# Optimization experiments

Measured on AMD Instinct MI355X. Metric: run time of the kernel, lower is better.

The kernel has to match this reference:

```python
import jax, jax.numpy as jnp
import numpy as np

D = 300   # hidden dim (Linear(300,300))
L = 160   # seq len, forced by W3 = Linear(160,1)


def _linear(x, W, b):
    # torch Linear: x @ W.T + b, W is (out, in)
    return jnp.matmul(x, W.T) + b


def setup_inputs() -> dict:
    key = jax.random.key(0)
    ks = jax.random.split(key, 16)
    B = 1024
    s = 1.0 / np.sqrt(D)
    inp = {
        'T_feature': jax.random.normal(ks[0], (B, L, D), jnp.float32),
        'CD_feature': jax.random.normal(ks[1], (B, L, D), jnp.float32),
        'Wproj': jax.random.normal(ks[2], (D, D), jnp.float32) * s,
        'bproj': jnp.zeros((D,), jnp.float32),
        'WqT_w': jax.random.normal(ks[3], (D, D), jnp.float32) * s,
        'WqT_b': jnp.zeros((D,), jnp.float32),
        'WqCD_w': jax.random.normal(ks[4], (D, D), jnp.float32) * s,
        'WqCD_b': jnp.zeros((D,), jnp.float32),
        'WkT_w': jax.random.normal(ks[5], (D, D), jnp.float32) * s,
        'WkT_b': jnp.zeros((D,), jnp.float32),
        'WkCD_w': jax.random.normal(ks[6], (D, D), jnp.float32) * s,
        'WkCD_b': jnp.zeros((D,), jnp.float32),
        'W3_w': jax.random.normal(ks[7], (1, L), jnp.float32) * (1.0 / np.sqrt(L)),
        'W3_b': jnp.zeros((1,), jnp.float32),
    }
    return inp


def reference(T_feature, CD_feature, Wproj, bproj, WqT_w, WqT_b, WqCD_w, WqCD_b,
              WkT_w, WkT_b, WkCD_w, WkCD_b, W3_w, W3_b):
    sqrt_d = jnp.sqrt(jnp.float32(D))
    proj_T = _linear(T_feature, Wproj, bproj)     # (B, L, D)
    proj_CD = _linear(CD_feature, Wproj, bproj)   # (B, L, D)

    # N_tensor @ proj_T is just the mean over tokens (weights 1/Len)
    mean_T = jnp.mean(proj_T, axis=1, keepdims=True)          # (B, 1, D)
    qT = _linear(mean_T, WqT_w, WqT_b)                        # (B, 1, D)
    kT = _linear(proj_T, WkT_w, WkT_b)                        # (B, L, D)
    alphaT = jnp.einsum('bqd,bkd->bqk', qT, kT) / sqrt_d      # (B, 1, L)
    ZT = jax.nn.sigmoid(alphaT)

    qCD = _linear(proj_CD, WqCD_w, WqCD_b)                    # (B, L, D)
    kCD = _linear(proj_CD, WkCD_w, WkCD_b)                    # (B, L, D)
    alphaCD = jnp.einsum('bqd,bkd->bqk', qCD, kCD) / sqrt_d   # (B, L, L)
    ZCD = jax.nn.sigmoid(alphaCD)

    # The per-token loop+cat is a plain broadcast multiply: Mt[:,i,:] = ZCD[:,i,:] * ZT[:,0,:]
    Mt = ZCD * ZT                                             # (B, L, L)
    alpha_f = jax.nn.softmax(_linear(Mt, W3_w, W3_b), axis=1) # (B, L, 1)

    # Second loop is a per-token scalar scale: HCD[:,i,:] = alpha_f[:,i,0] * proj_CD[:,i,:]
    HCD = alpha_f * proj_CD                                   # (B, L, D)
    return (proj_T, HCD)
```

## Files before the change

kernel.cpp:

```cpp
#include <hip/hip_runtime.h>
#include <hip/hip_bf16.h>


typedef __attribute__((ext_vector_type(8))) short short8;
typedef __attribute__((ext_vector_type(4))) float f32x4;

#define DP 320

__device__ __forceinline__ unsigned short f2bf(float x) {
  unsigned int u = __builtin_bit_cast(unsigned int, x);
  u += 0x7FFFu + ((u >> 16) & 1u);
  return (unsigned short)(u >> 16);
}
__device__ __forceinline__ float bf2f(unsigned short h) {
  unsigned int u = ((unsigned int)h) << 16;
  return __builtin_bit_cast(float, u);
}
__device__ __forceinline__ void gload16(const void* g, void* l) {
  __builtin_amdgcn_global_load_lds(
      (const __attribute__((address_space(1))) unsigned int*)g,
      (__attribute__((address_space(3))) unsigned int*)l, 16, 0, 0);
}
__device__ __forceinline__ float sigm(float x) { return 1.0f / (1.0f + __expf(-x)); }
__device__ __forceinline__ size_t baddr(int n, int k) {
  return (size_t)(k >> 6) * 20480 + (size_t)(n >> 4) * 1024 + ((k >> 5) & 1) * 512 +
         ((((k >> 3) & 3) << 4) | (n & 15)) * 8 + (k & 7);
}
__device__ __forceinline__ size_t aaddr(size_t r, int k) {
  return ((r >> 4) * 5 + (k >> 6)) * 1024 + ((k >> 5) & 1) * 512 +
         ((((k >> 3) & 3) << 4) | (r & 15)) * 8 + (k & 7);
}

__global__ __launch_bounds__(320)
void prep1_k(const float* __restrict__ W,
             const float* __restrict__ WqCD_w, const float* __restrict__ WqCD_b,
             const float* __restrict__ WkCD_w, const float* __restrict__ WkCD_b,
             const float* __restrict__ WqT_w, const float* __restrict__ WqT_b,
             const float* __restrict__ WkT_w, const float* __restrict__ WkT_b,
             unsigned short* __restrict__ Wb, float* __restrict__ Wt,
             unsigned short* __restrict__ MaugT, float* __restrict__ Pmat,
             float isd) {
  const int x = blockIdx.x, c = threadIdx.x;
  if (x < 320) {
    const int n = x;
    unsigned short v = (n < 300 && c < 300) ? f2bf(W[n * 300 + c]) : (unsigned short)0;
    Wb[baddr(n, c)] = v;
    if (n < 300 && c < 300) Wt[c * 304 + n] = W[n * 300 + c];
  } else if (x < 640) {
    const int n = x - 320;
    float v = 0.f;
    if (n <= 300 && c <= 300) {
      for (int o = 0; o < 300; ++o) {
        float a = (c < 300) ? WqCD_w[o * 300 + c] : WqCD_b[o];
        float b = (n < 300) ? WkCD_w[o * 300 + n] : WkCD_b[o];
        v += a * b;
      }
      v *= isd;
    }
    MaugT[baddr(n, c)] = f2bf(v);
  } else {
    const int n = x - 640;
    float v = 0.f;
    if (n <= 300 && c <= 300) {
      for (int o = 0; o < 300; ++o) {
        float a = (c < 300) ? WkT_w[o * 300 + c] : WkT_b[o];
        float b = (n < 300) ? WqT_w[o * 300 + n] : WqT_b[o];
        v += a * b;
      }
      v *= isd;
    }
    Pmat[n * DP + c] = v;
  }
}

__global__ __launch_bounds__(512)
void gemm_k(const float* __restrict__ Tf, const float* __restrict__ CDf,
            const unsigned short* __restrict__ Ah,
            const unsigned short* __restrict__ B01,
            const unsigned short* __restrict__ B2,
            const float* __restrict__ bias,
            float* __restrict__ Of, unsigned short* __restrict__ pCDout,
            unsigned short* __restrict__ Yout, int mode_base) {
  __shared__ __align__(16) unsigned short As[2][8192];
  __shared__ __align__(16) unsigned short Bs[2][20480];
  const int tid = threadIdx.x, wid = tid >> 6, lane = tid & 63;
  const int lr = lane & 15, hi = lane >> 4;
  const int wr = wid >> 2, wc = wid & 3;
  const int mode = mode_base + blockIdx.y;
  const size_t m0 = (size_t)blockIdx.x * 128;
  const unsigned short* __restrict__ Bm = (mode == 2) ? B2 : B01;
  const float* __restrict__ Af = (mode == 0) ? Tf : CDf;

  f32x4 acc[4][5];
#pragma unroll
  for (int i = 0; i < 4; ++i)
#pragma unroll
    for (int j = 0; j < 5; ++j) acc[i][j] = (f32x4){0.f, 0.f, 0.f, 0.f};

  f32x4 ar[4];
  auto loadA = [&](int kc) {
#pragma unroll
    for (int u = 0; u < 2; ++u) {
      const int unit = tid * 2 + u;
      const int row = unit >> 3, cg = unit & 7;
      const int col0 = kc * 64 + cg * 8;
      const float* p = Af + (m0 + row) * 300 + col0;
      if (col0 + 8 <= 300) {
        ar[u * 2] = *(const f32x4*)p;
        ar[u * 2 + 1] = *(const f32x4*)(p + 4);
      } else {
#pragma unroll
        for (int j = 0; j < 4; ++j) {
          ar[u * 2][j] = (col0 + j < 300) ? p[j] : 0.f;
          ar[u * 2 + 1][j] = (col0 + 4 + j < 300) ? p[4 + j] : 0.f;
        }
      }
    }
  };
  auto writeA = [&](int buf) {
#pragma unroll
    for (int u = 0; u < 2; ++u) {
      const int unit = tid * 2 + u;
      const int row = unit >> 3, cg = unit & 7;
      short8 h;
#pragma unroll
      for (int j = 0; j < 4; ++j) {
        h[j] = (short)f2bf(ar[u * 2][j]);
        h[j + 4] = (short)f2bf(ar[u * 2 + 1][j]);
      }
      *(short8*)&As[buf][(size_t)(row >> 4) * 1024 + (size_t)(cg >> 2) * 512 +
                         ((((cg & 3) << 4) | (row & 15)) * 8)] = h;
    }
  };
  auto stageA2 = [&](int buf, int kc) {
#pragma unroll
    for (int it = 0; it < 2; ++it) {
      int idx = it * 512 + tid;
      gload16(Ah + (((m0 >> 4) + (idx >> 7)) * 5 + kc) * 1024 + (size_t)(idx & 127) * 8,
              (char*)As[buf] + (size_t)idx * 16);
    }
  };
  auto stageB = [&](int buf, int kc) {
#pragma unroll
    for (int it = 0; it < 5; ++it) {
      int idx = it * 512 + tid;
      gload16(Bm + (size_t)kc * 20480 + (size_t)idx * 8, (char*)Bs[buf] + (size_t)idx * 16);
    }
  };

  if (mode < 2) { loadA(0); stageB(0, 0); writeA(0); }
  else { stageA2(0, 0); stageB(0, 0); }
  __syncthreads();

  for (int kc = 0; kc < 5; ++kc) {
    const int cur = kc & 1;
    if (kc < 4) {
      if (mode < 2) loadA(kc + 1);
      else stageA2(cur ^ 1, kc + 1);
      stageB(cur ^ 1, kc + 1);
    }
#pragma unroll
    for (int kk = 0; kk < 2; ++kk) {
      short8 a[4], b[5];
#pragma unroll
      for (int mf = 0; mf < 4; ++mf)
        a[mf] = *(const short8*)&As[cur][(size_t)(wr * 4 + mf) * 1024 + kk * 512 + lane * 8];
#pragma unroll
      for (int nf = 0; nf < 5; ++nf)
        b[nf] = *(const short8*)&Bs[cur][(size_t)(wc * 5 + nf) * 1024 + kk * 512 + lane * 8];
#pragma unroll
      for (int mf = 0; mf < 4; ++mf)
#pragma unroll
        for (int nf = 0; nf < 5; ++nf)
          acc[mf][nf] = __builtin_amdgcn_mfma_f32_16x16x32_bf16(a[mf], b[nf], acc[mf][nf], 0, 0, 0);
    }
    if (kc < 4 && mode < 2) writeA(cur ^ 1);
    __syncthreads();
  }

#pragma unroll
  for (int mf = 0; mf < 4; ++mf) {
    const size_t rowb = m0 + wr * 64 + mf * 16 + hi * 4;
#pragma unroll
    for (int nf = 0; nf < 5; ++nf) {
      const int col = wc * 80 + nf * 16 + lr;
      const float bv = (mode < 2) ? ((col < 300) ? bias[col] : 0.f) : 0.f;
#pragma unroll
      for (int r = 0; r < 4; ++r) {
        const size_t rw = rowb + r;
        float v = acc[mf][nf][r] + bv;
        if (mode == 0) {
          if (col < 300) Of[rw * 300 + col] = v;
        } else if (mode == 1) {
          unsigned short u = (col < 300) ? f2bf(v)
                           : ((col == 300) ? f2bf(1.0f) : (unsigned short)0);
          pCDout[aaddr(rw, col)] = u;
        } else {
          Yout[aaddr(rw, col)] = f2bf(v);
        }
      }
    }
  }
}

__global__ __launch_bounds__(320)
void gate2_k(const float* __restrict__ T, const float* __restrict__ Pmat,
             const float* __restrict__ W, const float* __restrict__ Wt,
             const float* __restrict__ bproj, float* __restrict__ ZT) {
  __shared__ float mt[304];
  __shared__ float maug[304];
  __shared__ float vv[304];
  __shared__ float wt[304];
  __shared__ float cpr;
  const int b = blockIdx.x, t = threadIdx.x;
  const int wid = t >> 6, lane = t & 63;
  const float* Tb = T + (size_t)b * 48000;
  if (t < 300) {
    float s = 0.f;
#pragma unroll 4
    for (int l = 0; l < 160; ++l) s += Tb[l * 300 + t];
    mt[t] = s * (1.0f / 160.0f);
  }
  __syncthreads();
  if (t < 304) {
    if (t < 300) {
      float s = 0.f;
      for (int o = 0; o < 300; ++o) s += Wt[o * 304 + t] * mt[o];
      maug[t] = s + bproj[t];
    } else maug[t] = (t == 300) ? 1.f : 0.f;
  }
  __syncthreads();
  if (t < 304) {
    float s = 0.f;
    if (t <= 300) for (int a = 0; a <= 300; ++a) s += Pmat[a * DP + t] * maug[a];
    vv[t] = s;
  }
  __syncthreads();
  if (t < 304) {
    if (t < 300) {
      float s = 0.f;
      for (int c = 0; c < 300; ++c) s += vv[c] * W[c * 300 + t];
      wt[t] = s;
    } else {
      wt[t] = 0.f;
      if (t == 300) {
        float s = 0.f;
        for (int c = 0; c < 300; ++c) s += vv[c] * bproj[c];
        cpr = s + vv[300];
      }
    }
  }
  __syncthreads();
  for (int j = wid * 32; j < wid * 32 + 32; ++j) {
    const float* row = Tb + j * 300;
    float s = 0.f;
    for (int c = lane; c < 300; c += 64) s += wt[c] * row[c];
#pragma unroll
    for (int m = 1; m < 64; m <<= 1) s += __shfl_xor(s, m, 64);
    if (lane == 0) ZT[b * 160 + j] = sigm(s + cpr);
  }
}

__global__ __launch_bounds__(640)
void finale_k(const unsigned short* __restrict__ Yg, const unsigned short* __restrict__ Pg,
              const float* __restrict__ ZT, const float* __restrict__ W3w,
              float* __restrict__ out) {
  __shared__ __align__(16) unsigned short Ps[51200];
  __shared__ float t_arr[160];
  __shared__ float s_arr[160];
  __shared__ float red0;
  const int b = blockIdx.x, tid = threadIdx.x, wid = tid >> 6, lane = tid & 63;
  const int lr = lane & 15, hi = lane >> 4;
  const unsigned short* Pb = Pg + (size_t)b * 51200;
  const unsigned short* Yb = Yg + (size_t)b * 51200;

  if (tid < 160) t_arr[tid] = ZT[b * 160 + tid] * W3w[tid];

  auto stageP = [&](int kc) {
#pragma unroll
    for (int it = 0; it < 2; ++it) {
      int idx = it * 640 + tid;
      int r16 = idx >> 7, rem = idx & 127;
      gload16(Pb + ((size_t)r16 * 5 + kc) * 1024 + (size_t)rem * 8,
              (char*)Ps + ((size_t)kc * 10240 + (size_t)idx * 8) * 2);
    }
  };
  short8 yf[2][2];
  auto loadY = [&](short8 (&dst)[2], int kc) {
#pragma unroll
    for (int kk = 0; kk < 2; ++kk)
      dst[kk] = *(const short8*)(Yb + ((size_t)wid * 5 + kc) * 1024 + kk * 512 + lane * 8);
  };

  f32x4 acc[10];
#pragma unroll
  for (int j = 0; j < 10; ++j) acc[j] = (f32x4){0.f, 0.f, 0.f, 0.f};

  stageP(0);
  loadY(yf[0], 0);
  __syncthreads();
#pragma unroll
  for (int kc = 0; kc < 5; ++kc) {
    const int cur = kc & 1;
    if (kc < 4) { stageP(kc + 1); loadY(yf[cur ^ 1], kc + 1); }
#pragma unroll
    for (int kk = 0; kk < 2; ++kk)
#pragma unroll
      for (int nf = 0; nf < 10; ++nf) {
        short8 bb = *(const short8*)&Ps[kc * 10240 + nf * 1024 + kk * 512 + lane * 8];
        acc[nf] = __builtin_amdgcn_mfma_f32_16x16x32_bf16(yf[cur][kk], bb, acc[nf], 0, 0, 0);
      }
    __syncthreads();
  }

  float pp[4];
#pragma unroll
  for (int r = 0; r < 4; ++r) {
    float s = 0.f;
#pragma unroll
    for (int nf = 0; nf < 10; ++nf) s += sigm(acc[nf][r]) * t_arr[nf * 16 + lr];
    pp[r] = s;
  }
#pragma unroll
  for (int m = 1; m < 16; m <<= 1)
#pragma unroll
    for (int r = 0; r < 4; ++r) pp[r] += __shfl_xor(pp[r], m, 64);
  if (lr == 0) {
#pragma unroll
    for (int r = 0; r < 4; ++r) s_arr[wid * 16 + hi * 4 + r] = pp[r];
  }
  __syncthreads();
  if (wid == 0) {
    float v0 = s_arr[lane], v1 = s_arr[lane + 64];
    float v2 = (lane < 32) ? s_arr[lane + 128] : -3.0e38f;
    float mx = fmaxf(fmaxf(v0, v1), v2);
#pragma unroll
    for (int m = 1; m < 64; m <<= 1) mx = fmaxf(mx, __shfl_xor(mx, m, 64));
    float e0 = __expf(v0 - mx), e1 = __expf(v1 - mx);
    float e2 = (lane < 32) ? __expf(v2 - mx) : 0.f;
    s_arr[lane] = e0; s_arr[lane + 64] = e1;
    if (lane < 32) s_arr[lane + 128] = e2;
    float sm = e0 + e1 + e2;
#pragma unroll
    for (int m = 1; m < 64; m <<= 1) sm += __shfl_xor(sm, m, 64);
    if (lane == 0) red0 = 1.0f / sm;
  }
  __syncthreads();
  const float inv = red0;
  float* ob = out + (size_t)b * 48000;
#pragma unroll
  for (int it = 0; it < 10; ++it) {
    int idx = it * 640 + tid;
    int i = idx / 40, g = idx - i * 40;
    int c0 = g * 8;
    if (c0 < 300) {
      short8 pv = *(const short8*)&Ps[(g >> 3) * 10240 + (i >> 4) * 1024 +
                                      ((g >> 2) & 1) * 512 + ((((g & 3) << 4) | (i & 15)) * 8)];
      float sc = s_arr[i] * inv;
      if (c0 + 8 <= 300) {
        f32x4 o0, o1;
#pragma unroll
        for (int j = 0; j < 4; ++j) { o0[j] = sc * bf2f((unsigned short)pv[j]); o1[j] = sc * bf2f((unsigned short)pv[j + 4]); }
        *(f32x4*)(ob + (size_t)i * 300 + c0) = o0;
        *(f32x4*)(ob + (size_t)i * 300 + c0 + 4) = o1;
      } else {
#pragma unroll
        for (int j = 0; j < 8; ++j) {
          int c = c0 + j;
          if (c < 300) ob[(size_t)i * 300 + c] = sc * bf2f((unsigned short)pv[j]);
        }
      }
    }
  }
}

extern "C" void kernel_launch(void* const* d_in, const int* in_sizes, int n_in,
                              void* d_out, int out_size, void* d_ws, size_t ws_size,
                              hipStream_t stream) {
  (void)in_sizes; (void)n_in; (void)out_size; (void)ws_size;
  const float* T      = (const float*)d_in[0];
  const float* CD     = (const float*)d_in[1];
  const float* Wproj  = (const float*)d_in[2];
  const float* bproj  = (const float*)d_in[3];
  const float* WqT_w  = (const float*)d_in[4];
  const float* WqT_b  = (const float*)d_in[5];
  const float* WqCD_w = (const float*)d_in[6];
  const float* WqCD_b = (const float*)d_in[7];
  const float* WkT_w  = (const float*)d_in[8];
  const float* WkT_b  = (const float*)d_in[9];
  const float* WkCD_w = (const float*)d_in[10];
  const float* WkCD_b = (const float*)d_in[11];
  const float* W3_w   = (const float*)d_in[12];

  char* ws = (char*)d_ws;
  size_t off = 0;
  auto alloc = [&](size_t bytes) { void* p = ws + off; off = (off + bytes + 255) & ~(size_t)255; return p; };
  unsigned short* Wb    = (unsigned short*)alloc((size_t)DP * DP * 2);
  unsigned short* MaugT = (unsigned short*)alloc((size_t)DP * DP * 2);
  float* Pmat = (float*)alloc((size_t)DP * DP * 4);
  float* Wt   = (float*)alloc((size_t)304 * 304 * 4);
  float* ZT   = (float*)alloc((size_t)1024 * 160 * 4);
  unsigned short* pCDg = (unsigned short*)alloc((size_t)163840 * DP * 2);
  unsigned short* Yg   = (unsigned short*)alloc((size_t)163840 * DP * 2);

  float* projT = (float*)d_out;
  float* HCD   = (float*)d_out + (size_t)49152000;

  const float isd = 1.0f / sqrtf(300.0f);

  prep1_k<<<dim3(960), dim3(320), 0, stream>>>(Wproj, WqCD_w, WqCD_b, WkCD_w, WkCD_b,
                                               WqT_w, WqT_b, WkT_w, WkT_b,
                                               Wb, Wt, MaugT, Pmat, isd);
  gemm_k<<<dim3(1280, 2), dim3(512), 0, stream>>>(T, CD, nullptr, Wb, nullptr,
                                                  bproj, projT, pCDg, nullptr, 0);
  gemm_k<<<dim3(1280, 1), dim3(512), 0, stream>>>(nullptr, nullptr, pCDg, nullptr, MaugT,
                                                  nullptr, nullptr, nullptr, Yg, 2);
  gate2_k<<<dim3(1024), dim3(320), 0, stream>>>(T, Pmat, Wproj, Wt, bproj, ZT);
  finale_k<<<dim3(1024), dim3(640), 0, stream>>>(Yg, pCDg, ZT, W3_w, HCD);
}
```

Measured before the change: 669.8 us.

## Shrink GEMM M-tile to 64 and load A fragments directly into registers

The GEMM block tile drops from 128 to 64 rows and the grid doubles. Each wave now loads its own A fragments straight from global memory into registers in MFMA layout instead of staging A through shared memory. This removes the A LDS buffer and its writes and reads, and sets launch_bounds to 4 blocks per CU to raise occupancy. In exchange, each B tile is reused across half as many rows, so B loads are repeated more often, and the uncoalesced per-lane A loads may waste bandwidth.

```diff
diff --git a/kernel.cpp b/kernel.cpp
--- a/kernel.cpp
+++ b/kernel.cpp
@@ -73,7 +73,7 @@
   }
 }
 
-__global__ __launch_bounds__(512)
+__global__ __launch_bounds__(512, 4)
 void gemm_k(const float* __restrict__ Tf, const float* __restrict__ CDf,
             const unsigned short* __restrict__ Ah,
             const unsigned short* __restrict__ B01,
@@ -81,63 +81,67 @@
             const float* __restrict__ bias,
             float* __restrict__ Of, unsigned short* __restrict__ pCDout,
             unsigned short* __restrict__ Yout, int mode_base) {
-  __shared__ __align__(16) unsigned short As[2][8192];
   __shared__ __align__(16) unsigned short Bs[2][20480];
   const int tid = threadIdx.x, wid = tid >> 6, lane = tid & 63;
   const int lr = lane & 15, hi = lane >> 4;
   const int wr = wid >> 2, wc = wid & 3;
   const int mode = mode_base + blockIdx.y;
-  const size_t m0 = (size_t)blockIdx.x * 128;
+  const size_t m0 = (size_t)blockIdx.x * 64;
   const unsigned short* __restrict__ Bm = (mode == 2) ? B2 : B01;
   const float* __restrict__ Af = (mode == 0) ? Tf : CDf;
 
-  f32x4 acc[4][5];
-#pragma unroll
-  for (int i = 0; i < 4; ++i)
+  f32x4 acc[2][5];
+#pragma unroll
+  for (int i = 0; i < 2; ++i)
 #pragma unroll
     for (int j = 0; j < 5; ++j) acc[i][j] = (f32x4){0.f, 0.f, 0.f, 0.f};
 
-  f32x4 ar[4];
-  auto loadA = [&](int kc) {
-#pragma unroll
-    for (int u = 0; u < 2; ++u) {
-      const int unit = tid * 2 + u;
-      const int row = unit >> 3, cg = unit & 7;
-      const int col0 = kc * 64 + cg * 8;
-      const float* p = Af + (m0 + row) * 300 + col0;
-      if (col0 + 8 <= 300) {
-        ar[u * 2] = *(const f32x4*)p;
-        ar[u * 2 + 1] = *(const f32x4*)(p + 4);
-      } else {
+  f32x4 ar[2][2][2];
+  short8 afc[2][2];
+  short8 afn[2][2];
+
+  auto loadA_f32 = [&](int kc) {
+#pragma unroll
+    for (int mf = 0; mf < 2; ++mf) {
+      const size_t row = m0 + wr * 32 + mf * 16 + lr;
+#pragma unroll
+      for (int kk = 0; kk < 2; ++kk) {
+        const int col0 = kc * 64 + kk * 32 + hi * 8;
+        const float* p = Af + row * 300 + col0;
+        if (col0 + 8 <= 300) {
+          ar[mf][kk][0] = *(const f32x4*)p;
+          ar[mf][kk][1] = *(const f32x4*)(p + 4);
+        } else {
+#pragma unroll
+          for (int j = 0; j < 4; ++j) {
+            ar[mf][kk][0][j] = (col0 + j < 300) ? p[j] : 0.f;
+            ar[mf][kk][1][j] = (col0 + 4 + j < 300) ? p[4 + j] : 0.f;
+          }
+        }
+      }
+    }
+  };
+  auto cvtA = [&]() {
+#pragma unroll
+    for (int mf = 0; mf < 2; ++mf)
+#pragma unroll
+      for (int kk = 0; kk < 2; ++kk) {
+        short8 h;
 #pragma unroll
         for (int j = 0; j < 4; ++j) {
-          ar[u * 2][j] = (col0 + j < 300) ? p[j] : 0.f;
-          ar[u * 2 + 1][j] = (col0 + 4 + j < 300) ? p[4 + j] : 0.f;
+          h[j] = (short)f2bf(ar[mf][kk][0][j]);
+          h[j + 4] = (short)f2bf(ar[mf][kk][1][j]);
         }
-      }
-    }
-  };
-  auto writeA = [&](int buf) {
-#pragma unroll
-    for (int u = 0; u < 2; ++u) {
-      const int unit = tid * 2 + u;
-      const int row = unit >> 3, cg = unit & 7;
-      short8 h;
-#pragma unroll
-      for (int j = 0; j < 4; ++j) {
-        h[j] = (short)f2bf(ar[u * 2][j]);
-        h[j + 4] = (short)f2bf(ar[u * 2 + 1][j]);
-      }
-      *(short8*)&As[buf][(size_t)(row >> 4) * 1024 + (size_t)(cg >> 2) * 512 +
-                         ((((cg & 3) << 4) | (row & 15)) * 8)] = h;
-    }
-  };
-  auto stageA2 = [&](int buf, int kc) {
-#pragma unroll
-    for (int it = 0; it < 2; ++it) {
-      int idx = it * 512 + tid;
-      gload16(Ah + (((m0 >> 4) + (idx >> 7)) * 5 + kc) * 1024 + (size_t)(idx & 127) * 8,
-              (char*)As[buf] + (size_t)idx * 16);
+        afc[mf][kk] = h;
+      }
+  };
+  auto loadA_h = [&](short8 (&dst)[2][2], int kc) {
+#pragma unroll
+    for (int mf = 0; mf < 2; ++mf) {
+      const size_t rt = (m0 >> 4) + wr * 2 + mf;
+#pragma unroll
+      for (int kk = 0; kk < 2; ++kk)
+        dst[mf][kk] = *(const short8*)(Ah + (rt * 5 + kc) * 1024 + kk * 512 + lane * 8);
     }
   };
   auto stageB = [&](int buf, int kc) {
@@ -148,39 +152,44 @@
     }
   };
 
-  if (mode < 2) { loadA(0); stageB(0, 0); writeA(0); }
-  else { stageA2(0, 0); stageB(0, 0); }
+  if (mode < 2) { loadA_f32(0); stageB(0, 0); cvtA(); }
+  else { loadA_h(afc, 0); stageB(0, 0); }
   __syncthreads();
 
   for (int kc = 0; kc < 5; ++kc) {
     const int cur = kc & 1;
     if (kc < 4) {
-      if (mode < 2) loadA(kc + 1);
-      else stageA2(cur ^ 1, kc + 1);
+      if (mode < 2) loadA_f32(kc + 1);
+      else loadA_h(afn, kc + 1);
       stageB(cur ^ 1, kc + 1);
     }
 #pragma unroll
     for (int kk = 0; kk < 2; ++kk) {
-      short8 a[4], b[5];
-#pragma unroll
-      for (int mf = 0; mf < 4; ++mf)
-        a[mf] = *(const short8*)&As[cur][(size_t)(wr * 4 + mf) * 1024 + kk * 512 + lane * 8];
+      short8 b[5];
 #pragma unroll
       for (int nf = 0; nf < 5; ++nf)
         b[nf] = *(const short8*)&Bs[cur][(size_t)(wc * 5 + nf) * 1024 + kk * 512 + lane * 8];
 #pragma unroll
-      for (int mf = 0; mf < 4; ++mf)
+      for (int mf = 0; mf < 2; ++mf)
 #pragma unroll
         for (int nf = 0; nf < 5; ++nf)
-          acc[mf][nf] = __builtin_amdgcn_mfma_f32_16x16x32_bf16(a[mf], b[nf], acc[mf][nf], 0, 0, 0);
-    }
-    if (kc < 4 && mode < 2) writeA(cur ^ 1);
+          acc[mf][nf] = __builtin_amdgcn_mfma_f32_16x16x32_bf16(afc[mf][kk], b[nf], acc[mf][nf], 0, 0, 0);
+    }
+    if (kc < 4) {
+      if (mode < 2) cvtA();
+      else {
+#pragma unroll
+        for (int mf = 0; mf < 2; ++mf)
+#pragma unroll
+          for (int kk = 0; kk < 2; ++kk) afc[mf][kk] = afn[mf][kk];
+      }
+    }
     __syncthreads();
   }
 
 #pragma unroll
-  for (int mf = 0; mf < 4; ++mf) {
-    const size_t rowb = m0 + wr * 64 + mf * 16 + hi * 4;
+  for (int mf = 0; mf < 2; ++mf) {
+    const size_t rowb = m0 + wr * 32 + mf * 16 + hi * 4;
 #pragma unroll
     for (int nf = 0; nf < 5; ++nf) {
       const int col = wc * 80 + nf * 16 + lr;
@@ -411,9 +420,9 @@
   prep1_k<<<dim3(960), dim3(320), 0, stream>>>(Wproj, WqCD_w, WqCD_b, WkCD_w, WkCD_b,
                                                WqT_w, WqT_b, WkT_w, WkT_b,
                                                Wb, Wt, MaugT, Pmat, isd);
-  gemm_k<<<dim3(1280, 2), dim3(512), 0, stream>>>(T, CD, nullptr, Wb, nullptr,
+  gemm_k<<<dim3(2560, 2), dim3(512), 0, stream>>>(T, CD, nullptr, Wb, nullptr,
                                                   bproj, projT, pCDg, nullptr, 0);
-  gemm_k<<<dim3(1280, 1), dim3(512), 0, stream>>>(nullptr, nullptr, pCDg, nullptr, MaugT,
+  gemm_k<<<dim3(2560, 1), dim3(512), 0, stream>>>(nullptr, nullptr, pCDg, nullptr, MaugT,
                                                   nullptr, nullptr, nullptr, Yg, 2);
   gate2_k<<<dim3(1024), dim3(320), 0, stream>>>(T, Pmat, Wproj, Wt, bproj, ZT);
   finale_k<<<dim3(1024), dim3(640), 0, stream>>>(Yg, pCDg, ZT, W3_w, HCD);
```

After: 1.467 ms. 119% more time.
